# Optimization experiments

Hardware: AMD Instinct MI355X
Metric: run time of the kernel (lower is better)

Reference implementation:

```python
import jax, jax.numpy as jnp
import numpy as np

TIME_WEIGHT = 0.1
CURRENT_TIME = 0.0

def setup_inputs() -> dict:
    key = jax.random.key(0)
    k1, k2, k3, k4, k5 = jax.random.split(key, 5)
    B, M, D, C = 131072, 100, 1024, 16
    return {
        "query": jax.random.normal(k1, (B, D), dtype=jnp.float32),
        "context": jax.random.normal(k2, (B, C), dtype=jnp.float32),
        "mem_keys": jax.random.normal(k3, (M, D), dtype=jnp.float32),
        "mem_values": jax.random.normal(k4, (M, D), dtype=jnp.float32),
        "mem_contexts": jax.random.normal(k5, (M, C), dtype=jnp.float32),
        "mem_timestamps": jnp.zeros((M, 1), dtype=jnp.float32),
    }

def reference(query, context, mem_keys, mem_values, mem_contexts, mem_timestamps):
    # content scores: [B, M]
    scores = jnp.einsum('bd,md->bm', query, mem_keys)
    # contextual binding
    scores = scores + 0.5 * jnp.einsum('bc,mc->bm', context, mem_contexts)
    # exponential time-decay bias, broadcast over batch: [M]
    time_decay = jnp.exp(-TIME_WEIGHT * (CURRENT_TIME - mem_timestamps.squeeze(-1)))
    scores = scores + time_decay[None, :]
    attn = jax.nn.softmax(scores, axis=-1)
    return jnp.einsum('bm,md->bd', attn, mem_values)
```

## Files before the change

kernel.cpp:

```cpp
#include <hip/hip_runtime.h>


typedef __attribute__((ext_vector_type(8))) _Float16 f16x8;
typedef __attribute__((ext_vector_type(4))) float f32x4;

constexpr int DQ = 1024, CD = 16, MM = 100, KD = 1056, NT = 7;
constexpr int VROW = 144;
constexpr size_t KE = (size_t)112 * KD;

constexpr int QBUF = 16384, KOFF = 49152, KBUF = 7168;
constexpr int VOFF = 43008, VBUF = 9216, PW = 8192;
constexpr int LDSZ = 70656;

#define WAITV(n) asm volatile("s_waitcnt vmcnt(" #n ")" ::: "memory")

__device__ __forceinline__ void gl16(const void* g, void* l) {
    __builtin_amdgcn_global_load_lds(
        (const __attribute__((address_space(1))) unsigned int*)g,
        (__attribute__((address_space(3))) unsigned int*)l, 16, 0, 0);
}

__global__ void build_k(const float* __restrict__ mk, const float* __restrict__ mc,
                        _Float16* __restrict__ KH)
{
    int d = blockIdx.x * 64 + threadIdx.x;
    int m = blockIdx.y;
    if (d >= KD) return;
    float x = 0.f;
    if (m < MM) {
        if (d < DQ)            x = mk[(size_t)m * DQ + d];
        else if (d < DQ + CD)  x = 0.5f * mc[(size_t)m * CD + (d - DQ)];
    }
    KH[(size_t)m * KD + d] = (_Float16)x;
}

__global__ void build_vt(const float* __restrict__ mv, _Float16* __restrict__ VT)
{
    int d = blockIdx.x;
    int m = threadIdx.x;
    if (m < VROW)
        VT[(size_t)d * VROW + m] = (m < MM) ? (_Float16)mv[(size_t)m * DQ + d] : (_Float16)0.f;
}

__global__ __launch_bounds__(256, 2)
void epmem_pipe(const float* __restrict__ q, const float* __restrict__ cx,
                const float* __restrict__ ts,
                const _Float16* __restrict__ KH, const _Float16* __restrict__ VT,
                float* __restrict__ out)
{
    __shared__ __align__(16) char lds[LDSZ];

    const int t = threadIdx.x, w = t >> 6, lane = t & 63;
    const int lr = lane & 15, lk = lane >> 4;
    const int row0 = blockIdx.x * 128;

    auto stageQ = [&](int buf, int ks) {
        char* dst = lds + buf * QBUF;
        #pragma unroll
        for (int rd = 0; rd < 4; ++rd) {
            int s = rd * 256 + w * 64 + lane;
            int slotg = (s & 7) ^ ((s >> 4) & 3);
            gl16(q + (size_t)(row0 + (s >> 3)) * DQ + ks * 32 + slotg * 4,
                 dst + (rd * 256 + w * 64) * 16);
        }
    };
    auto stageQctx = [&](int buf) {
        char* dst = lds + buf * QBUF;
        #pragma unroll
        for (int rd = 0; rd < 2; ++rd) {
            int s = rd * 256 + w * 64 + lane;
            gl16(cx + (size_t)(row0 + (s >> 2)) * CD + (s & 3) * 4,
                 dst + (rd * 256 + w * 64) * 16);
        }
    };
    auto stageK = [&](int buf, int ks) {
        char* dst = lds + KOFF + buf * KBUF;
        {
            int s = w * 64 + lane;
            gl16(KH + (size_t)(s >> 2) * KD + ks * 32 + (s & 3) * 8, dst + (w * 64) * 16);
        }
        if (w < 3) {
            int s = 256 + w * 64 + lane;
            gl16(KH + (size_t)(s >> 2) * KD + ks * 32 + (s & 3) * 8, dst + (256 + w * 64) * 16);
        }
    };
    auto stageV = [&](int buf, int c) {
        char* dst = lds + VOFF + buf * VBUF;
        const char* src = (const char*)(VT + (size_t)c * 32 * VROW);
        for (int rd = w; rd < 9; rd += 4)
            gl16(src + (rd * 64 + lane) * 16, dst + rd * 1024);
    };

    f32x4 acc[2][NT];
    #pragma unroll
    for (int rt = 0; rt < 2; ++rt)
        #pragma unroll
        for (int nt = 0; nt < NT; ++nt) acc[rt][nt] = (f32x4){0.f, 0.f, 0.f, 0.f};

    stageQ(0, 0); stageK(0, 0);
    stageQ(1, 1); stageK(1, 1);
    if (w < 3) { WAITV(6); } else { WAITV(5); }
    __builtin_amdgcn_s_barrier();

    int bc = 0, bs = 2;
    for (int ks = 0; ks <= 32; ++ks) {
        if (ks + 2 <= 32) {
            if (ks + 2 == 32) stageQctx(bs); else stageQ(bs, ks + 2);
            stageK(bs, ks + 2);
        }
        const char* qb = lds + bc * QBUF;
        f16x8 ah[2], al[2];
        if (ks < 32) {
            const int g = (lr >> 1) & 3;
            #pragma unroll
            for (int rt = 0; rt < 2; ++rt) {
                const char* base = qb + (w * 32 + rt * 16 + lr) * 128;
                f32x4 x = *(const f32x4*)(base + (((2 * lk)     ^ g) << 4));
                f32x4 y = *(const f32x4*)(base + (((2 * lk + 1) ^ g) << 4));
                #pragma unroll
                for (int e = 0; e < 4; ++e) {
                    _Float16 h = (_Float16)x[e]; ah[rt][e] = h;     al[rt][e] = (_Float16)(x[e] - (float)h);
                    h = (_Float16)y[e];          ah[rt][4 + e] = h; al[rt][4 + e] = (_Float16)(y[e] - (float)h);
                }
            }
        } else {
            #pragma unroll
            for (int rt = 0; rt < 2; ++rt) {
                if (lk < 2) {
                    const float* qr = (const float*)qb + (w * 32 + rt * 16 + lr) * 16 + lk * 8;
                    f32x4 x = *(const f32x4*)qr, y = *(const f32x4*)(qr + 4);
                    #pragma unroll
                    for (int e = 0; e < 4; ++e) {
                        _Float16 h = (_Float16)x[e]; ah[rt][e] = h;     al[rt][e] = (_Float16)(x[e] - (float)h);
                        h = (_Float16)y[e];          ah[rt][4 + e] = h; al[rt][4 + e] = (_Float16)(y[e] - (float)h);
                    }
                } else {
                    #pragma unroll
                    for (int e = 0; e < 8; ++e) { ah[rt][e] = (_Float16)0.f; al[rt][e] = (_Float16)0.f; }
                }
            }
        }
        #pragma unroll
        for (int nt = 0; nt < NT; ++nt) {
            f16x8 bh = *(const f16x8*)(lds + KOFF + bc * KBUF + ((nt * 16 + lr) * 32 + lk * 8) * 2);
            acc[0][nt] = __builtin_amdgcn_mfma_f32_16x16x32_f16(ah[0], bh, acc[0][nt], 0, 0, 0);
            acc[0][nt] = __builtin_amdgcn_mfma_f32_16x16x32_f16(al[0], bh, acc[0][nt], 0, 0, 0);
            acc[1][nt] = __builtin_amdgcn_mfma_f32_16x16x32_f16(ah[1], bh, acc[1][nt], 0, 0, 0);
            acc[1][nt] = __builtin_amdgcn_mfma_f32_16x16x32_f16(al[1], bh, acc[1][nt], 0, 0, 0);
        }
        if (ks < 30)       { if (w < 3) { WAITV(6); } else { WAITV(5); } }
        else if (ks == 30) { if (w < 3) { WAITV(4); } else { WAITV(3); } }
        else if (ks == 31) { WAITV(0); }
        if (ks < 32) __builtin_amdgcn_s_barrier();
        bc = (bc == 2) ? 0 : bc + 1;
        bs = (bs == 2) ? 0 : bs + 1;
    }

    asm volatile("" ::: "memory");
    __builtin_amdgcn_s_barrier();
    stageV(0, 0); stageV(1, 1);

    float dec[NT];
    #pragma unroll
    for (int nt = 0; nt < NT; ++nt) {
        int m = nt * 16 + lr;
        dec[nt] = (m < MM) ? __expf(0.1f * ts[m]) : 0.f;
    }
    _Float16* Pw = (_Float16*)(lds + w * PW);
    #pragma unroll
    for (int rt = 0; rt < 2; ++rt) {
        float rm[4] = {-3e38f, -3e38f, -3e38f, -3e38f};
        #pragma unroll
        for (int nt = 0; nt < NT; ++nt) {
            int m = nt * 16 + lr;
            #pragma unroll
            for (int r = 0; r < 4; ++r) {
                float s = (m < MM) ? (acc[rt][nt][r] + dec[nt]) : -3e38f;
                acc[rt][nt][r] = s;
                rm[r] = fmaxf(rm[r], s);
            }
        }
        #pragma unroll
        for (int r = 0; r < 4; ++r)
            #pragma unroll
            for (int off = 1; off < 16; off <<= 1)
                rm[r] = fmaxf(rm[r], __shfl_xor(rm[r], off));
        float rs[4] = {0.f, 0.f, 0.f, 0.f};
        #pragma unroll
        for (int nt = 0; nt < NT; ++nt)
            #pragma unroll
            for (int r = 0; r < 4; ++r) {
                float e = __expf(acc[rt][nt][r] - rm[r]);
                acc[rt][nt][r] = e;
                rs[r] += e;
            }
        #pragma unroll
        for (int r = 0; r < 4; ++r)
            #pragma unroll
            for (int off = 1; off < 16; off <<= 1)
                rs[r] += __shfl_xor(rs[r], off);
        float inv[4];
        #pragma unroll
        for (int r = 0; r < 4; ++r) inv[r] = 1.f / rs[r];
        #pragma unroll
        for (int nt = 0; nt < NT; ++nt)
            #pragma unroll
            for (int r = 0; r < 4; ++r)
                Pw[(16 * rt + 4 * lk + r) * 128 + nt * 16 + lr] = (_Float16)(acc[rt][nt][r] * inv[r]);
    }
    {
        int row = lane & 31, half = lane >> 5;
        uint4 z = {0u, 0u, 0u, 0u};
        *(uint4*)(lds + w * PW + (row * 128 + 112 + half * 8) * 2) = z;
    }
    if (w == 0) { WAITV(3); } else { WAITV(2); }
    __builtin_amdgcn_s_barrier();

    f16x8 pa[2][4];
    #pragma unroll
    for (int rt = 0; rt < 2; ++rt)
        #pragma unroll
        for (int k4 = 0; k4 < 4; ++k4)
            pa[rt][k4] = *(const f16x8*)(lds + w * PW + ((rt * 16 + lr) * 128 + k4 * 32 + lk * 8) * 2);

    int vc = 0, vs = 2;
    for (int c = 0; c < 32; ++c) {
        if (c + 2 < 32) stageV(vs, c + 2);
        f32x4 o[2][2];
        #pragma unroll
        for (int rt = 0; rt < 2; ++rt)
            #pragma unroll
            for (int n2 = 0; n2 < 2; ++n2) o[rt][n2] = (f32x4){0.f, 0.f, 0.f, 0.f};
        #pragma unroll
        for (int k4 = 0; k4 < 4; ++k4) {
            #pragma unroll
            for (int n2 = 0; n2 < 2; ++n2) {
                f16x8 bv = *(const f16x8*)(lds + VOFF + vc * VBUF
                              + ((n2 * 16 + lr) * VROW + k4 * 32 + lk * 8) * 2);
                o[0][n2] = __builtin_amdgcn_mfma_f32_16x16x32_f16(pa[0][k4], bv, o[0][n2], 0, 0, 0);
                o[1][n2] = __builtin_amdgcn_mfma_f32_16x16x32_f16(pa[1][k4], bv, o[1][n2], 0, 0, 0);
            }
        }
        #pragma unroll
        for (int rt = 0; rt < 2; ++rt)
            #pragma unroll
            for (int n2 = 0; n2 < 2; ++n2) {
                const int col = c * 32 + n2 * 16 + lr;
                #pragma unroll
                for (int r = 0; r < 4; ++r)
                    out[(size_t)(row0 + w * 32 + rt * 16 + 4 * lk + r) * DQ + col] = o[rt][n2][r];
            }
        if (c < 30)       { if (w == 0) { WAITV(19); } else { WAITV(18); } }
        else if (c == 30) { WAITV(16); }
        if (c < 31) __builtin_amdgcn_s_barrier();
        vc = (vc == 2) ? 0 : vc + 1;
        vs = (vs == 2) ? 0 : vs + 1;
    }
}

extern "C" void kernel_launch(void* const* d_in, const int* in_sizes, int n_in,
                              void* d_out, int out_size, void* d_ws, size_t ws_size,
                              hipStream_t stream) {
    const float* q  = (const float*)d_in[0];
    const float* cx = (const float*)d_in[1];
    const float* mk = (const float*)d_in[2];
    const float* mv = (const float*)d_in[3];
    const float* mc = (const float*)d_in[4];
    const float* ts = (const float*)d_in[5];
    float* out = (float*)d_out;

    _Float16* wsp = (_Float16*)d_ws;
    _Float16* KH = wsp;
    _Float16* VT = wsp + KE;

    const int B = in_sizes[0] / DQ;

    build_k<<<dim3(17, 112), dim3(64), 0, stream>>>(mk, mc, KH);
    build_vt<<<dim3(1024), dim3(256), 0, stream>>>(mv, VT);
    epmem_pipe<<<dim3(B / 128), dim3(256), 0, stream>>>(q, cx, ts, KH, VT, out);
}
```

Measured before the change: 306.0 us.

## Split 128-row tile across 8 waves with XOR-swizzled LDS layouts

Each block now runs 512 threads (8 waves, 16 rows each) instead of 4 waves with 32 rows, which halves per-wave accumulator registers and raises occupancy via launch_bounds(512,4). The V-transpose row stride changes from 144 to 128 halves, and Q, K, V and P LDS tiles gain XOR swizzles to avoid bank conflicts. Staging and vmcnt wait counts are reworked for the new per-wave load counts. The risk is more barrier traffic per block and fragile hand-tuned waitcnt values.

```diff
diff --git a/kernel.cpp b/kernel.cpp
--- a/kernel.cpp
+++ b/kernel.cpp
@@ -5,11 +5,10 @@
 typedef __attribute__((ext_vector_type(4))) float f32x4;
 
 constexpr int DQ = 1024, CD = 16, MM = 100, KD = 1056, NT = 7;
-constexpr int VROW = 144;
 constexpr size_t KE = (size_t)112 * KD;
 
 constexpr int QBUF = 16384, KOFF = 49152, KBUF = 7168;
-constexpr int VOFF = 43008, VBUF = 9216, PW = 8192;
+constexpr int VOFF = 32768, VBUF = 8192;
 constexpr int LDSZ = 70656;
 
 #define WAITV(n) asm volatile("s_waitcnt vmcnt(" #n ")" ::: "memory")
@@ -36,13 +35,12 @@
 
 __global__ void build_vt(const float* __restrict__ mv, _Float16* __restrict__ VT)
 {
-    int d = blockIdx.x;
-    int m = threadIdx.x;
-    if (m < VROW)
-        VT[(size_t)d * VROW + m] = (m < MM) ? (_Float16)mv[(size_t)m * DQ + d] : (_Float16)0.f;
-}
-
-__global__ __launch_bounds__(256, 2)
+    int idx = blockIdx.x * 256 + threadIdx.x;
+    int d = idx >> 7, m = idx & 127;
+    VT[idx] = (m < MM) ? (_Float16)mv[(size_t)m * DQ + d] : (_Float16)0.f;
+}
+
+__global__ __launch_bounds__(512, 4)
 void epmem_pipe(const float* __restrict__ q, const float* __restrict__ cx,
                 const float* __restrict__ ts,
                 const _Float16* __restrict__ KH, const _Float16* __restrict__ VT,
@@ -54,129 +52,114 @@
     const int lr = lane & 15, lk = lane >> 4;
     const int row0 = blockIdx.x * 128;
 
-    auto stageQ = [&](int buf, int ks) {
-        char* dst = lds + buf * QBUF;
-        #pragma unroll
-        for (int rd = 0; rd < 4; ++rd) {
-            int s = rd * 256 + w * 64 + lane;
-            int slotg = (s & 7) ^ ((s >> 4) & 3);
-            gl16(q + (size_t)(row0 + (s >> 3)) * DQ + ks * 32 + slotg * 4,
-                 dst + (rd * 256 + w * 64) * 16);
-        }
-    };
-    auto stageQctx = [&](int buf) {
-        char* dst = lds + buf * QBUF;
-        #pragma unroll
-        for (int rd = 0; rd < 2; ++rd) {
-            int s = rd * 256 + w * 64 + lane;
-            gl16(cx + (size_t)(row0 + (s >> 2)) * CD + (s & 3) * 4,
-                 dst + (rd * 256 + w * 64) * 16);
-        }
-    };
-    auto stageK = [&](int buf, int ks) {
-        char* dst = lds + KOFF + buf * KBUF;
-        {
-            int s = w * 64 + lane;
-            gl16(KH + (size_t)(s >> 2) * KD + ks * 32 + (s & 3) * 8, dst + (w * 64) * 16);
-        }
-        if (w < 3) {
-            int s = 256 + w * 64 + lane;
-            gl16(KH + (size_t)(s >> 2) * KD + ks * 32 + (s & 3) * 8, dst + (256 + w * 64) * 16);
-        }
-    };
-    auto stageV = [&](int buf, int c) {
-        char* dst = lds + VOFF + buf * VBUF;
-        const char* src = (const char*)(VT + (size_t)c * 32 * VROW);
-        for (int rd = w; rd < 9; rd += 4)
-            gl16(src + (rd * 64 + lane) * 16, dst + rd * 1024);
-    };
-
-    f32x4 acc[2][NT];
-    #pragma unroll
-    for (int rt = 0; rt < 2; ++rt)
-        #pragma unroll
-        for (int nt = 0; nt < NT; ++nt) acc[rt][nt] = (f32x4){0.f, 0.f, 0.f, 0.f};
-
-    stageQ(0, 0); stageK(0, 0);
-    stageQ(1, 1); stageK(1, 1);
-    if (w < 3) { WAITV(6); } else { WAITV(5); }
-    __builtin_amdgcn_s_barrier();
-
-    int bc = 0, bs = 2;
-    for (int ks = 0; ks <= 32; ++ks) {
-        if (ks + 2 <= 32) {
-            if (ks + 2 == 32) stageQctx(bs); else stageQ(bs, ks + 2);
-            stageK(bs, ks + 2);
-        }
-        const char* qb = lds + bc * QBUF;
-        f16x8 ah[2], al[2];
-        if (ks < 32) {
-            const int g = (lr >> 1) & 3;
-            #pragma unroll
-            for (int rt = 0; rt < 2; ++rt) {
-                const char* base = qb + (w * 32 + rt * 16 + lr) * 128;
-                f32x4 x = *(const f32x4*)(base + (((2 * lk)     ^ g) << 4));
-                f32x4 y = *(const f32x4*)(base + (((2 * lk + 1) ^ g) << 4));
-                #pragma unroll
-                for (int e = 0; e < 4; ++e) {
-                    _Float16 h = (_Float16)x[e]; ah[rt][e] = h;     al[rt][e] = (_Float16)(x[e] - (float)h);
-                    h = (_Float16)y[e];          ah[rt][4 + e] = h; al[rt][4 + e] = (_Float16)(y[e] - (float)h);
-                }
-            }
-        } else {
-            #pragma unroll
-            for (int rt = 0; rt < 2; ++rt) {
-                if (lk < 2) {
-                    const float* qr = (const float*)qb + (w * 32 + rt * 16 + lr) * 16 + lk * 8;
-                    f32x4 x = *(const f32x4*)qr, y = *(const f32x4*)(qr + 4);
-                    #pragma unroll
-                    for (int e = 0; e < 4; ++e) {
-                        _Float16 h = (_Float16)x[e]; ah[rt][e] = h;     al[rt][e] = (_Float16)(x[e] - (float)h);
-                        h = (_Float16)y[e];          ah[rt][4 + e] = h; al[rt][4 + e] = (_Float16)(y[e] - (float)h);
-                    }
-                } else {
-                    #pragma unroll
-                    for (int e = 0; e < 8; ++e) { ah[rt][e] = (_Float16)0.f; al[rt][e] = (_Float16)0.f; }
-                }
-            }
-        }
-        #pragma unroll
-        for (int nt = 0; nt < NT; ++nt) {
-            f16x8 bh = *(const f16x8*)(lds + KOFF + bc * KBUF + ((nt * 16 + lr) * 32 + lk * 8) * 2);
-            acc[0][nt] = __builtin_amdgcn_mfma_f32_16x16x32_f16(ah[0], bh, acc[0][nt], 0, 0, 0);
-            acc[0][nt] = __builtin_amdgcn_mfma_f32_16x16x32_f16(al[0], bh, acc[0][nt], 0, 0, 0);
-            acc[1][nt] = __builtin_amdgcn_mfma_f32_16x16x32_f16(ah[1], bh, acc[1][nt], 0, 0, 0);
-            acc[1][nt] = __builtin_amdgcn_mfma_f32_16x16x32_f16(al[1], bh, acc[1][nt], 0, 0, 0);
-        }
-        if (ks < 30)       { if (w < 3) { WAITV(6); } else { WAITV(5); } }
-        else if (ks == 30) { if (w < 3) { WAITV(4); } else { WAITV(3); } }
-        else if (ks == 31) { WAITV(0); }
-        if (ks < 32) __builtin_amdgcn_s_barrier();
-        bc = (bc == 2) ? 0 : bc + 1;
-        bs = (bs == 2) ? 0 : bs + 1;
-    }
-
-    asm volatile("" ::: "memory");
-    __builtin_amdgcn_s_barrier();
-    stageV(0, 0); stageV(1, 1);
-
     float dec[NT];
     #pragma unroll
     for (int nt = 0; nt < NT; ++nt) {
         int m = nt * 16 + lr;
         dec[nt] = (m < MM) ? __expf(0.1f * ts[m]) : 0.f;
     }
-    _Float16* Pw = (_Float16*)(lds + w * PW);
+
+    auto stageQ = [&](int buf, int ks) {
+        char* dst = lds + buf * QBUF;
+        #pragma unroll
+        for (int i = 0; i < 2; ++i) {
+            int s = i * 512 + w * 64 + lane;
+            int row = s >> 3;
+            int logical = (s & 7) ^ (row & 7);
+            gl16(q + (size_t)(row0 + row) * DQ + ks * 32 + logical * 4,
+                 dst + (i * 512 + w * 64) * 16);
+        }
+    };
+    auto stageQctx = [&](int buf) {
+        char* dst = lds + buf * QBUF;
+        gl16(cx + (size_t)(row0 + (t >> 2)) * CD + (t & 3) * 4, dst + (w * 64) * 16);
+    };
+    auto stageK = [&](int buf, int ks) {
+        if (w < 7) {
+            char* dst = lds + KOFF + buf * KBUF;
+            int s = w * 64 + lane;
+            int m = s >> 2;
+            int logical = (s & 3) ^ ((m >> 1) & 3);
+            gl16(KH + (size_t)m * KD + ks * 32 + logical * 8, dst + (w * 64) * 16);
+        }
+    };
+    auto stageV = [&](int buf, int c) {
+        char* dst = lds + VOFF + buf * VBUF;
+        int d = t >> 4;
+        int logical = (t & 15) ^ (d & 15);
+        gl16(VT + (size_t)(c * 32 + d) * 128 + logical * 8, dst + (w * 64) * 16);
+    };
+
+    f32x4 acc[NT];
     #pragma unroll
-    for (int rt = 0; rt < 2; ++rt) {
-        float rm[4] = {-3e38f, -3e38f, -3e38f, -3e38f};
+    for (int nt = 0; nt < NT; ++nt) acc[nt] = (f32x4){0.f, 0.f, 0.f, 0.f};
+
+    stageQ(0, 0); stageK(0, 0);
+    stageQ(1, 1); stageK(1, 1);
+    if (w < 7) { WAITV(3); } else { WAITV(2); }
+    __builtin_amdgcn_s_barrier();
+
+    int bc = 0;
+    for (int ks = 0; ks <= 32; ++ks) {
+        int bs = bc + 2; if (bs >= 3) bs -= 3;
+        if (ks + 2 < 32)       { stageQ(bs, ks + 2); stageK(bs, ks + 2); }
+        else if (ks + 2 == 32) { stageQctx(bs);      stageK(bs, 32); }
+
+        const char* qb = lds + bc * QBUF;
+        f16x8 ah, al;
+        if (ks < 32) {
+            const char* base = qb + (w * 16 + lr) * 128;
+            const int g = lr & 7;
+            f32x4 x = *(const f32x4*)(base + (((2 * lk)     ^ g) << 4));
+            f32x4 y = *(const f32x4*)(base + (((2 * lk + 1) ^ g) << 4));
+            #pragma unroll
+            for (int e = 0; e < 4; ++e) {
+                _Float16 h = (_Float16)x[e]; ah[e] = h;     al[e] = (_Float16)(x[e] - (float)h);
+                h = (_Float16)y[e];          ah[4 + e] = h; al[4 + e] = (_Float16)(y[e] - (float)h);
+            }
+        } else {
+            if (lk < 2) {
+                const char* base = qb + (w * 16 + lr) * 64;
+                f32x4 x = *(const f32x4*)(base + (2 * lk) * 16);
+                f32x4 y = *(const f32x4*)(base + (2 * lk + 1) * 16);
+                #pragma unroll
+                for (int e = 0; e < 4; ++e) {
+                    _Float16 h = (_Float16)x[e]; ah[e] = h;     al[e] = (_Float16)(x[e] - (float)h);
+                    h = (_Float16)y[e];          ah[4 + e] = h; al[4 + e] = (_Float16)(y[e] - (float)h);
+                }
+            } else {
+                #pragma unroll
+                for (int e = 0; e < 8; ++e) { ah[e] = (_Float16)0.f; al[e] = (_Float16)0.f; }
+            }
+        }
         #pragma unroll
         for (int nt = 0; nt < NT; ++nt) {
             int m = nt * 16 + lr;
+            f16x8 bh = *(const f16x8*)(lds + KOFF + bc * KBUF
+                         + ((m << 2) + (lk ^ ((lr >> 1) & 3))) * 16);
+            acc[nt] = __builtin_amdgcn_mfma_f32_16x16x32_f16(ah, bh, acc[nt], 0, 0, 0);
+            acc[nt] = __builtin_amdgcn_mfma_f32_16x16x32_f16(al, bh, acc[nt], 0, 0, 0);
+        }
+        if (ks <= 29)      { if (w < 7) { WAITV(3); } else { WAITV(2); } }
+        else if (ks == 30) { if (w < 7) { WAITV(2); } else { WAITV(1); } }
+        else if (ks == 31) { WAITV(0); }
+        if (ks < 32) __builtin_amdgcn_s_barrier();
+        if (++bc == 3) bc = 0;
+    }
+
+    __builtin_amdgcn_s_barrier();
+    stageV(0, 0); stageV(1, 1);
+
+    char* Pb = lds + w * 4096;
+    {
+        float rm[4] = {-3e38f, -3e38f, -3e38f, -3e38f};
+        #pragma unroll
+        for (int nt = 0; nt < NT; ++nt) {
+            int m = nt * 16 + lr;
             #pragma unroll
             for (int r = 0; r < 4; ++r) {
-                float s = (m < MM) ? (acc[rt][nt][r] + dec[nt]) : -3e38f;
-                acc[rt][nt][r] = s;
+                float s = (m < MM) ? (acc[nt][r] + dec[nt]) : -3e38f;
+                acc[nt][r] = s;
                 rm[r] = fmaxf(rm[r], s);
             }
         }
@@ -190,8 +173,8 @@
         for (int nt = 0; nt < NT; ++nt)
             #pragma unroll
             for (int r = 0; r < 4; ++r) {
-                float e = __expf(acc[rt][nt][r] - rm[r]);
-                acc[rt][nt][r] = e;
+                float e = __expf(acc[nt][r] - rm[r]);
+                acc[nt][r] = e;
                 rs[r] += e;
             }
         #pragma unroll
@@ -199,62 +182,53 @@
             #pragma unroll
             for (int off = 1; off < 16; off <<= 1)
                 rs[r] += __shfl_xor(rs[r], off);
-        float inv[4];
-        #pragma unroll
-        for (int r = 0; r < 4; ++r) inv[r] = 1.f / rs[r];
-        #pragma unroll
-        for (int nt = 0; nt < NT; ++nt)
-            #pragma unroll
-            for (int r = 0; r < 4; ++r)
-                Pw[(16 * rt + 4 * lk + r) * 128 + nt * 16 + lr] = (_Float16)(acc[rt][nt][r] * inv[r]);
-    }
-    {
-        int row = lane & 31, half = lane >> 5;
+        #pragma unroll
+        for (int r = 0; r < 4; ++r) {
+            float inv = 1.f / rs[r];
+            int row = 4 * lk + r;
+            #pragma unroll
+            for (int nt = 0; nt < NT; ++nt)
+                *(_Float16*)(Pb + row * 256 + (((nt * 2 + (lr >> 3)) ^ row) & 15) * 16
+                             + (lr & 7) * 2) = (_Float16)(acc[nt][r] * inv);
+        }
+    }
+    if (lane < 32) {
+        int row = lane >> 1, sl = 14 + (lane & 1);
         uint4 z = {0u, 0u, 0u, 0u};
-        *(uint4*)(lds + w * PW + (row * 128 + 112 + half * 8) * 2) = z;
-    }
-    if (w == 0) { WAITV(3); } else { WAITV(2); }
+        *(uint4*)(Pb + row * 256 + ((sl ^ row) & 15) * 16) = z;
+    }
+    WAITV(1);
     __builtin_amdgcn_s_barrier();
 
-    f16x8 pa[2][4];
+    f16x8 pa[4];
     #pragma unroll
-    for (int rt = 0; rt < 2; ++rt)
-        #pragma unroll
-        for (int k4 = 0; k4 < 4; ++k4)
-            pa[rt][k4] = *(const f16x8*)(lds + w * PW + ((rt * 16 + lr) * 128 + k4 * 32 + lk * 8) * 2);
-
-    int vc = 0, vs = 2;
+    for (int k4 = 0; k4 < 4; ++k4)
+        pa[k4] = *(const f16x8*)(Pb + lr * 256 + (((k4 * 4 + lk) ^ lr) & 15) * 16);
+
+    int vc = 0;
     for (int c = 0; c < 32; ++c) {
+        int vs = vc + 2; if (vs >= 3) vs -= 3;
         if (c + 2 < 32) stageV(vs, c + 2);
-        f32x4 o[2][2];
-        #pragma unroll
-        for (int rt = 0; rt < 2; ++rt)
-            #pragma unroll
-            for (int n2 = 0; n2 < 2; ++n2) o[rt][n2] = (f32x4){0.f, 0.f, 0.f, 0.f};
+        f32x4 o0 = {0.f, 0.f, 0.f, 0.f}, o1 = {0.f, 0.f, 0.f, 0.f};
         #pragma unroll
         for (int k4 = 0; k4 < 4; ++k4) {
-            #pragma unroll
-            for (int n2 = 0; n2 < 2; ++n2) {
-                f16x8 bv = *(const f16x8*)(lds + VOFF + vc * VBUF
-                              + ((n2 * 16 + lr) * VROW + k4 * 32 + lk * 8) * 2);
-                o[0][n2] = __builtin_amdgcn_mfma_f32_16x16x32_f16(pa[0][k4], bv, o[0][n2], 0, 0, 0);
-                o[1][n2] = __builtin_amdgcn_mfma_f32_16x16x32_f16(pa[1][k4], bv, o[1][n2], 0, 0, 0);
-            }
-        }
-        #pragma unroll
-        for (int rt = 0; rt < 2; ++rt)
-            #pragma unroll
-            for (int n2 = 0; n2 < 2; ++n2) {
-                const int col = c * 32 + n2 * 16 + lr;
-                #pragma unroll
-                for (int r = 0; r < 4; ++r)
-                    out[(size_t)(row0 + w * 32 + rt * 16 + 4 * lk + r) * DQ + col] = o[rt][n2][r];
-            }
-        if (c < 30)       { if (w == 0) { WAITV(19); } else { WAITV(18); } }
+            const char* vb = lds + VOFF + vc * VBUF + (((k4 * 4 + lk) ^ lr) & 15) * 16;
+            f16x8 b0 = *(const f16x8*)(vb + lr * 256);
+            f16x8 b1 = *(const f16x8*)(vb + (16 + lr) * 256);
+            o0 = __builtin_amdgcn_mfma_f32_16x16x32_f16(pa[k4], b0, o0, 0, 0, 0);
+            o1 = __builtin_amdgcn_mfma_f32_16x16x32_f16(pa[k4], b1, o1, 0, 0, 0);
+        }
+        #pragma unroll
+        for (int r = 0; r < 4; ++r) {
+            size_t rw = (size_t)(row0 + w * 16 + 4 * lk + r) * DQ + c * 32;
+            out[rw + lr]      = o0[r];
+            out[rw + 16 + lr] = o1[r];
+        }
+        if (c == 0)       { WAITV(9); }
+        else if (c <= 29) { WAITV(17); }
         else if (c == 30) { WAITV(16); }
         if (c < 31) __builtin_amdgcn_s_barrier();
-        vc = (vc == 2) ? 0 : vc + 1;
-        vs = (vs == 2) ? 0 : vs + 1;
+        if (++vc == 3) vc = 0;
     }
 }
 
@@ -276,6 +250,6 @@
     const int B = in_sizes[0] / DQ;
 
     build_k<<<dim3(17, 112), dim3(64), 0, stream>>>(mk, mc, KH);
-    build_vt<<<dim3(1024), dim3(256), 0, stream>>>(mv, VT);
-    epmem_pipe<<<dim3(B / 128), dim3(256), 0, stream>>>(q, cx, ts, KH, VT, out);
-}
+    build_vt<<<dim3(512), dim3(256), 0, stream>>>(mv, VT);
+    epmem_pipe<<<dim3(B / 128), dim3(512), 0, stream>>>(q, cx, ts, KH, VT, out);
+}
```

Result: no change. 306.3 us (+0.1%).
